# Optimization experiments

Hardware: AMD Instinct MI355X
Metric: run time of the kernel (lower is better)

The kernel has to match this reference:

```python
import jax, jax.numpy as jnp
import numpy as np

NUM_AGES = 100
FEAT_DIM = 512
BATCH = 4096
TEMPERATURE = 0.1
EPS = 1e-6


def setup_inputs() -> dict:
    key = jax.random.key(0)
    k1, k2, k3 = jax.random.split(key, 3)
    z_age = jax.random.normal(k1, (BATCH, FEAT_DIM), dtype=jnp.float32)
    ages = jax.random.randint(k2, (BATCH,), 0, NUM_AGES, dtype=jnp.int64)
    proxies = jax.random.normal(k3, (NUM_AGES, FEAT_DIM), dtype=jnp.float32)
    return {"z_age": z_age, "ages": ages, "proxies": proxies}


def _unit_diff(a, b):
    d = a - b
    return d / (jnp.linalg.norm(d, axis=-1, keepdims=True) + EPS)


def reference(z_age, ages, proxies):
    # Vectorized equivalent of the O(B^2) python double loop.
    # Only pairs with age_i < age_j contribute (age_i > age_j branch is a no-op `...`).
    B = z_age.shape[0]
    A = proxies.shape[0]
    aj = ages.astype(jnp.int32)
    c_cur = proxies[aj]                                   # [B, D]
    c_next = proxies[jnp.minimum(aj + 1, A - 1)]          # [B, D]
    c_prev = proxies[jnp.maximum(aj - 1, 0)]              # [B, D]
    vf = _unit_diff(c_next, c_cur)                        # forward direction per sample j
    vb = _unit_diff(c_prev, c_cur)                        # backward direction per sample j

    # Pairwise norms via Gram matrix: ||z_i - z_j||.
    G = z_age @ z_age.T                                   # [B, B]
    sq = jnp.diagonal(G)                                  # [B]
    d2 = jnp.maximum(sq[:, None] + sq[None, :] - 2.0 * G, 0.0)
    norm = jnp.sqrt(d2)                                   # [B, B]
    denom = norm + EPS

    # dot(v_d_ij, v_f_j) = (z_i . vf_j - z_j . vf_j) / (||z_i - z_j|| + eps)
    Gf = z_age @ vf.T                                     # [B, B], Gf[i, j] = z_i . vf_j
    Gb = z_age @ vb.T
    dot_f = (Gf - jnp.diagonal(Gf)[None, :]) / denom
    dot_b = (Gb - jnp.diagonal(Gb)[None, :]) / denom

    # -log(exp(df/T) / (exp(df/T) + exp(db/T))) = softplus((db - df)/T)
    per_pair = jax.nn.softplus((dot_b - dot_f) / TEMPERATURE)  # [B, B]
    mask = ages[:, None] < ages[None, :]
    loss = jnp.sum(jnp.where(mask, per_pair, 0.0))
    return loss / (B * (B - 1))
```

## Files before the change

kernel.cpp:

```cpp
#include <hip/hip_runtime.h>
#include <hip/hip_bf16.h>

#define NUM_AGES 100
#define FEAT 512
#define BATCH 4096
#define EPSF 1e-6f
#define INV_T 10.0f

#define BM 128
#define BN 64
#define BK 32
#define GRID_N (BATCH / BN)
#define GRID_M (BATCH / BM)

typedef __bf16 bf16_t;
typedef __bf16 v8bf __attribute__((ext_vector_type(8)));
typedef float v4f __attribute__((ext_vector_type(4)));

__device__ __forceinline__ void async16(const void* g, void* l) {
  __builtin_amdgcn_global_load_lds(
      (const __attribute__((address_space(1))) void*)g,
      (__attribute__((address_space(3))) void*)l, 16, 0, 0);
}

__global__ __launch_bounds__(256) void prep_kernel(
    const float* __restrict__ z, const int* __restrict__ ages,
    const float* __restrict__ proxies,
    bf16_t* __restrict__ zb, bf16_t* __restrict__ wb,
    float* __restrict__ sq, float* __restrict__ hd)
{
  int j = blockIdx.x;
  int t = threadIdx.x;
  int a = ages[j];
  if (a < 0) a = 0;
  if (a > NUM_AGES - 1) a = NUM_AGES - 1;
  const float* cc = proxies + (size_t)a * FEAT;
  const float* cn = proxies + (size_t)(a + 1 > NUM_AGES - 1 ? NUM_AGES - 1 : a + 1) * FEAT;
  const float* cp = proxies + (size_t)(a - 1 < 0 ? 0 : a - 1) * FEAT;
  const float* zr = z + (size_t)j * FEAT;

  float zf[2], dff[2], dbf[2];
  float s_ff = 0.f, s_bb = 0.f, s_zz = 0.f, s_zf = 0.f, s_zb = 0.f;
#pragma unroll
  for (int e = 0; e < 2; ++e) {
    int c = t + e * 256;
    float ccv = cc[c];
    dff[e] = cn[c] - ccv;
    dbf[e] = cp[c] - ccv;
    zf[e] = zr[c];
    s_ff += dff[e] * dff[e];
    s_bb += dbf[e] * dbf[e];
    s_zz += zf[e] * zf[e];
    s_zf += zf[e] * dff[e];
    s_zb += zf[e] * dbf[e];
  }
#pragma unroll
  for (int off = 32; off > 0; off >>= 1) {
    s_ff += __shfl_down(s_ff, off, 64);
    s_bb += __shfl_down(s_bb, off, 64);
    s_zz += __shfl_down(s_zz, off, 64);
    s_zf += __shfl_down(s_zf, off, 64);
    s_zb += __shfl_down(s_zb, off, 64);
  }
  __shared__ float red[4][5];
  int wv = t >> 6, lane = t & 63;
  if (lane == 0) {
    red[wv][0] = s_ff; red[wv][1] = s_bb; red[wv][2] = s_zz;
    red[wv][3] = s_zf; red[wv][4] = s_zb;
  }
  __syncthreads();
  float ff = red[0][0] + red[1][0] + red[2][0] + red[3][0];
  float bb = red[0][1] + red[1][1] + red[2][1] + red[3][1];
  float zz = red[0][2] + red[1][2] + red[2][2] + red[3][2];
  float zdf = red[0][3] + red[1][3] + red[2][3] + red[3][3];
  float zdb = red[0][4] + red[1][4] + red[2][4] + red[3][4];

  float rf = 1.0f / (sqrtf(ff) + EPSF);
  float rb = 1.0f / (sqrtf(bb) + EPSF);
#pragma unroll
  for (int e = 0; e < 2; ++e) {
    int c = t + e * 256;
    float wval = dbf[e] * rb - dff[e] * rf;
    wb[(size_t)j * FEAT + c] = (bf16_t)wval;
    zb[(size_t)j * FEAT + c] = (bf16_t)zf[e];
  }
  if (t == 0) {
    sq[j] = zz;
    hd[j] = rb * zdb - rf * zdf;
  }
}

__global__ __launch_bounds__(256, 3) void pair_kernel(
    const bf16_t* __restrict__ zb, const bf16_t* __restrict__ wb,
    const float* __restrict__ sq, const float* __restrict__ hd,
    const int* __restrict__ ages, float* __restrict__ partial)
{
  __shared__ __attribute__((aligned(16))) char lds[16384];
  __shared__ float s_sqi[BM];
  __shared__ int   s_agei[BM];
  __shared__ float s_sqj[BN];
  __shared__ float s_hdj[BN];
  __shared__ int   s_agej[BN];
  __shared__ float wsum[4];

  int t = threadIdx.x;
  int wv = t >> 6, lane = t & 63;
  int i0 = blockIdx.y * BM, j0 = blockIdx.x * BN;

  if (t < BM) {
    s_sqi[t] = sq[i0 + t];
    s_agei[t] = ages[i0 + t];
  } else if (t < BM + BN) {
    int u = t - BM;
    s_sqj[u] = sq[j0 + u];
    s_hdj[u] = hd[j0 + u];
    s_agej[u] = ages[j0 + u];
  }

  v4f accG[4][2], accH[4][2];
#pragma unroll
  for (int a = 0; a < 4; ++a)
#pragma unroll
    for (int b = 0; b < 2; ++b) {
      accG[a][b] = (v4f){0.f, 0.f, 0.f, 0.f};
      accH[a][b] = (v4f){0.f, 0.f, 0.f, 0.f};
    }

  int wm = wv >> 1, wn = wv & 1;
  int lm = lane & 15, q = lane >> 4;

  int grow = lane >> 2;
  int gcol = (lane & 3) * 8;

  const bf16_t* pA0 = zb + (size_t)(i0 + wv * 16 + grow) * FEAT + gcol;
  const bf16_t* pA1 = zb + (size_t)(i0 + 64 + wv * 16 + grow) * FEAT + gcol;
  const bf16_t* pZ  = zb + (size_t)(j0 + wv * 16 + grow) * FEAT + gcol;
  const bf16_t* pW  = wb + (size_t)(j0 + wv * 16 + grow) * FEAT + gcol;
  char* dA0 = lds + wv * 1024;
  char* dA1 = lds + 4096 + wv * 1024;
  char* dZ  = lds + 8192 + wv * 1024;
  char* dW  = lds + 12288 + wv * 1024;

  for (int k0 = 0; k0 < FEAT; k0 += BK) {
    async16(pA0, dA0);
    async16(pA1, dA1);
    async16(pZ, dZ);
    async16(pW, dW);
    pA0 += BK; pA1 += BK; pZ += BK; pW += BK;
    __syncthreads();

    v8bf afr[4], bz[2], bw[2];
#pragma unroll
    for (int mi = 0; mi < 4; ++mi) {
      int r = wm * 64 + mi * 16 + lm;
      afr[mi] = *(const v8bf*)(lds + r * 64 + q * 16);
    }
#pragma unroll
    for (int ni = 0; ni < 2; ++ni) {
      int r = wn * 32 + ni * 16 + lm;
      bz[ni] = *(const v8bf*)(lds + 8192 + r * 64 + q * 16);
      bw[ni] = *(const v8bf*)(lds + 12288 + r * 64 + q * 16);
    }
#pragma unroll
    for (int mi = 0; mi < 4; ++mi)
#pragma unroll
      for (int ni = 0; ni < 2; ++ni) {
        accG[mi][ni] = __builtin_amdgcn_mfma_f32_16x16x32_bf16(afr[mi], bz[ni], accG[mi][ni], 0, 0, 0);
        accH[mi][ni] = __builtin_amdgcn_mfma_f32_16x16x32_bf16(afr[mi], bw[ni], accH[mi][ni], 0, 0, 0);
      }
    __syncthreads();
  }

  float tsum = 0.f;
#pragma unroll
  for (int ni = 0; ni < 2; ++ni) {
    int jl = wn * 32 + ni * 16 + lm;
    float sqj = s_sqj[jl];
    float hdj = s_hdj[jl];
    int aj = s_agej[jl];
#pragma unroll
    for (int mi = 0; mi < 4; ++mi) {
#pragma unroll
      for (int r = 0; r < 4; ++r) {
        int il = wm * 64 + mi * 16 + q * 4 + r;
        float g = accG[mi][ni][r];
        float h = accH[mi][ni][r];
        float d2 = fmaxf(s_sqi[il] + sqj - 2.0f * g, 1e-12f);
        float rs = __builtin_amdgcn_rsqf(d2);
        float arg = (h - hdj) * INV_T * rs;
        float sp = fmaxf(arg, 0.0f) + __logf(1.0f + __expf(-fabsf(arg)));
        tsum += (s_agei[il] < aj) ? sp : 0.0f;
      }
    }
  }

#pragma unroll
  for (int off = 32; off > 0; off >>= 1) tsum += __shfl_down(tsum, off, 64);
  if (lane == 0) wsum[wv] = tsum;
  __syncthreads();
  if (t == 0)
    partial[blockIdx.y * gridDim.x + blockIdx.x] = wsum[0] + wsum[1] + wsum[2] + wsum[3];
}

__global__ __launch_bounds__(256) void reduce_kernel(
    const float* __restrict__ partial, int n, float* __restrict__ out)
{
  int t = threadIdx.x;
  double s = 0.0;
  for (int idx = t; idx < n; idx += 256) s += (double)partial[idx];
#pragma unroll
  for (int off = 32; off > 0; off >>= 1) s += __shfl_down(s, off, 64);
  __shared__ double ws[4];
  int wv = t >> 6, lane = t & 63;
  if (lane == 0) ws[wv] = s;
  __syncthreads();
  if (t == 0) {
    double tot = ws[0] + ws[1] + ws[2] + ws[3];
    out[0] = (float)(tot / ((double)BATCH * (double)(BATCH - 1)));
  }
}

extern "C" void kernel_launch(void* const* d_in, const int* in_sizes, int n_in,
                              void* d_out, int out_size, void* d_ws, size_t ws_size,
                              hipStream_t stream) {
  const float* z = (const float*)d_in[0];
  const int* ages = (const int*)d_in[1];
  const float* proxies = (const float*)d_in[2];
  float* out = (float*)d_out;

  char* ws = (char*)d_ws;
  bf16_t* zb = (bf16_t*)ws;
  bf16_t* wb = (bf16_t*)(ws + (size_t)4 * 1024 * 1024);
  float* sq = (float*)(ws + (size_t)8 * 1024 * 1024);
  float* hd = (float*)(ws + (size_t)8 * 1024 * 1024 + 16384);
  float* partial = (float*)(ws + (size_t)8 * 1024 * 1024 + 32768);

  prep_kernel<<<BATCH, 256, 0, stream>>>(z, ages, proxies, zb, wb, sq, hd);
  dim3 grid(GRID_N, GRID_M);
  pair_kernel<<<grid, 256, 0, stream>>>(zb, wb, sq, hd, ages, partial);
  reduce_kernel<<<1, 256, 0, stream>>>(partial, GRID_N * GRID_M, out);
}
```

Before: 119.0 us.

## Sort samples by age and launch only upper-triangular pair tiles

Adds a counting-sort kernel that orders samples by age, and permutes the prep outputs into that order. Because only pairs with age_i < age_j contribute, tiles entirely below the diagonal of the sorted order can be skipped. The pair kernel therefore launches a 1D grid of upper-triangular tiles decoded with a small loop. This roughly halves the GEMM and epilogue work, at the cost of an extra single-block sort launch and a gather in prep.

```diff
diff --git a/kernel.cpp b/kernel.cpp
--- a/kernel.cpp
+++ b/kernel.cpp
@@ -10,8 +10,7 @@
 #define BM 128
 #define BN 64
 #define BK 32
-#define GRID_N (BATCH / BN)
-#define GRID_M (BATCH / BM)
+#define NTILES 1056
 
 typedef __bf16 bf16_t;
 typedef __bf16 v8bf __attribute__((ext_vector_type(8)));
@@ -23,21 +22,49 @@
       (__attribute__((address_space(3))) void*)l, 16, 0, 0);
 }
 
+__global__ __launch_bounds__(1024) void sort_kernel(
+    const int* __restrict__ ages, int* __restrict__ perm)
+{
+  __shared__ int hist[NUM_AGES];
+  __shared__ int base[NUM_AGES];
+  int t = threadIdx.x;
+  if (t < NUM_AGES) hist[t] = 0;
+  __syncthreads();
+  for (int j = t; j < BATCH; j += 1024) {
+    int a = ages[j];
+    a = a < 0 ? 0 : (a > NUM_AGES - 1 ? NUM_AGES - 1 : a);
+    atomicAdd(&hist[a], 1);
+  }
+  __syncthreads();
+  if (t == 0) {
+    int s = 0;
+    for (int a = 0; a < NUM_AGES; ++a) { base[a] = s; s += hist[a]; }
+  }
+  __syncthreads();
+  for (int j = t; j < BATCH; j += 1024) {
+    int a = ages[j];
+    a = a < 0 ? 0 : (a > NUM_AGES - 1 ? NUM_AGES - 1 : a);
+    int pos = atomicAdd(&base[a], 1);
+    perm[pos] = j;
+  }
+}
+
 __global__ __launch_bounds__(256) void prep_kernel(
     const float* __restrict__ z, const int* __restrict__ ages,
-    const float* __restrict__ proxies,
+    const float* __restrict__ proxies, const int* __restrict__ perm,
     bf16_t* __restrict__ zb, bf16_t* __restrict__ wb,
-    float* __restrict__ sq, float* __restrict__ hd)
+    float* __restrict__ sq, float* __restrict__ hd,
+    int* __restrict__ ages_s)
 {
   int j = blockIdx.x;
-  int t = threadIdx.x;
-  int a = ages[j];
-  if (a < 0) a = 0;
-  if (a > NUM_AGES - 1) a = NUM_AGES - 1;
+  int s = perm[j];
+  int t = threadIdx.x;
+  int araw = ages[s];
+  int a = araw < 0 ? 0 : (araw > NUM_AGES - 1 ? NUM_AGES - 1 : araw);
   const float* cc = proxies + (size_t)a * FEAT;
   const float* cn = proxies + (size_t)(a + 1 > NUM_AGES - 1 ? NUM_AGES - 1 : a + 1) * FEAT;
   const float* cp = proxies + (size_t)(a - 1 < 0 ? 0 : a - 1) * FEAT;
-  const float* zr = z + (size_t)j * FEAT;
+  const float* zr = z + (size_t)s * FEAT;
 
   float zf[2], dff[2], dbf[2];
   float s_ff = 0.f, s_bb = 0.f, s_zz = 0.f, s_zf = 0.f, s_zb = 0.f;
@@ -87,6 +114,7 @@
   if (t == 0) {
     sq[j] = zz;
     hd[j] = rb * zdb - rf * zdf;
+    ages_s[j] = araw;
   }
 }
 
@@ -105,7 +133,12 @@
 
   int t = threadIdx.x;
   int wv = t >> 6, lane = t & 63;
-  int i0 = blockIdx.y * BM, j0 = blockIdx.x * BN;
+
+  int rem = blockIdx.x;
+  int by = 0;
+  while (rem >= 64 - 2 * by) { rem -= 64 - 2 * by; ++by; }
+  int bx = 2 * by + rem;
+  int i0 = by * BM, j0 = bx * BN;
 
   if (t < BM) {
     s_sqi[t] = sq[i0 + t];
@@ -199,7 +232,7 @@
   if (lane == 0) wsum[wv] = tsum;
   __syncthreads();
   if (t == 0)
-    partial[blockIdx.y * gridDim.x + blockIdx.x] = wsum[0] + wsum[1] + wsum[2] + wsum[3];
+    partial[blockIdx.x] = wsum[0] + wsum[1] + wsum[2] + wsum[3];
 }
 
 __global__ __launch_bounds__(256) void reduce_kernel(
@@ -231,12 +264,15 @@
   char* ws = (char*)d_ws;
   bf16_t* zb = (bf16_t*)ws;
   bf16_t* wb = (bf16_t*)(ws + (size_t)4 * 1024 * 1024);
-  float* sq = (float*)(ws + (size_t)8 * 1024 * 1024);
-  float* hd = (float*)(ws + (size_t)8 * 1024 * 1024 + 16384);
-  float* partial = (float*)(ws + (size_t)8 * 1024 * 1024 + 32768);
-
-  prep_kernel<<<BATCH, 256, 0, stream>>>(z, ages, proxies, zb, wb, sq, hd);
-  dim3 grid(GRID_N, GRID_M);
-  pair_kernel<<<grid, 256, 0, stream>>>(zb, wb, sq, hd, ages, partial);
-  reduce_kernel<<<1, 256, 0, stream>>>(partial, GRID_N * GRID_M, out);
-}
+  size_t o = (size_t)8 * 1024 * 1024;
+  float* sq      = (float*)(ws + o);
+  float* hd      = (float*)(ws + o + 16384);
+  float* partial = (float*)(ws + o + 32768);
+  int*   perm    = (int*)  (ws + o + 49152);
+  int*   ages_s  = (int*)  (ws + o + 65536);
+
+  sort_kernel<<<1, 1024, 0, stream>>>(ages, perm);
+  prep_kernel<<<BATCH, 256, 0, stream>>>(z, ages, proxies, perm, zb, wb, sq, hd, ages_s);
+  pair_kernel<<<NTILES, 256, 0, stream>>>(zb, wb, sq, hd, ages_s, partial);
+  reduce_kernel<<<1, 256, 0, stream>>>(partial, NTILES, out);
+}
```

Result: faster. 108.7 us (-8.6%).
